# Kernel tuning notes

Measured on AMD Instinct MI355X. Metric: run time of the kernel, lower is better.

Reference implementation:

```python
import jax, jax.numpy as jnp
import numpy as np

IN_DIM = 512
HID = 512
NUM_PARENTS = 200000


def setup_inputs() -> dict:
    key = jax.random.key(0)
    k0, k1, k2, k3, k4 = jax.random.split(key, 5)
    s = 1.0 / np.sqrt(HID)
    return {
        "parent_states": jax.random.normal(k0, (NUM_PARENTS, IN_DIM), dtype=jnp.float32),
        # torch.nn.GRUCell parameters: weight_ih (3H, D), weight_hh (3H, H), biases (3H,)
        "weight_ih": jax.random.uniform(k1, (3 * HID, IN_DIM), minval=-s, maxval=s, dtype=jnp.float32),
        "weight_hh": jax.random.uniform(k2, (3 * HID, HID), minval=-s, maxval=s, dtype=jnp.float32),
        "bias_ih": jax.random.uniform(k3, (3 * HID,), minval=-s, maxval=s, dtype=jnp.float32),
        "bias_hh": jax.random.uniform(k4, (3 * HID,), minval=-s, maxval=s, dtype=jnp.float32),
    }


def reference(parent_states, weight_ih, weight_hh, bias_ih, bias_hh):
    # 1) permutation-invariant aggregation of parent states (mean)
    agg = jnp.mean(parent_states, axis=0)  # (IN_DIM,)
    # 2) GRUCell update with hx = zeros (torch GRUCell default when hx is None)
    h = jnp.zeros((HID,), dtype=parent_states.dtype)
    gi = weight_ih @ agg + bias_ih          # (3H,)
    gh = weight_hh @ h + bias_hh            # (3H,) -> just bias_hh since h=0
    gi_r, gi_z, gi_n = jnp.split(gi, 3)
    gh_r, gh_z, gh_n = jnp.split(gh, 3)
    r = jax.nn.sigmoid(gi_r + gh_r)
    z = jax.nn.sigmoid(gi_z + gh_z)
    n = jnp.tanh(gi_n + r * gh_n)
    h_new = (1.0 - z) * n + z * h           # (HID,)
    return h_new
```

## Files before the change

### kernel.cpp

```cpp
#include <hip/hip_runtime.h>
#include <math.h>

#define IN_DIM 512
#define HID 512

#define K1_BLOCKS 1024
#define K1_THREADS 256
#define K1_STRIDE (K1_BLOCKS * K1_THREADS)
#define P1 K1_BLOCKS
#define K2_BLOCKS 64
#define P2 K2_BLOCKS

__global__ __launch_bounds__(K1_THREADS) void k1_partial(const float* __restrict__ x,
                                                         float* __restrict__ part,
                                                         int total4) {
    const int gtid = blockIdx.x * K1_THREADS + threadIdx.x;
    const float4* __restrict__ x4 = (const float4*)x;
    float4 acc = make_float4(0.f, 0.f, 0.f, 0.f);
    for (int i = gtid; i < total4; i += K1_STRIDE) {
        float4 v = x4[i];
        acc.x += v.x; acc.y += v.y; acc.z += v.z; acc.w += v.w;
    }
    __shared__ float4 lds[K1_THREADS];
    lds[threadIdx.x] = acc;
    __syncthreads();
    if (threadIdx.x < 128) {
        float4 a = lds[threadIdx.x];
        float4 b = lds[threadIdx.x + 128];
        float4 s = make_float4(a.x + b.x, a.y + b.y, a.z + b.z, a.w + b.w);
        ((float4*)(part + (size_t)blockIdx.x * IN_DIM))[threadIdx.x] = s;
    }
}

__global__ __launch_bounds__(IN_DIM) void k2_reduce(const float* __restrict__ part,
                                                    float* __restrict__ part2) {
    const int j = threadIdx.x;
    const int g = blockIdx.x;
    float s = 0.f;
    const int rows = P1 / P2;
    const float* __restrict__ base = part + (size_t)g * rows * IN_DIM + j;
    for (int r = 0; r < rows; ++r) s += base[(size_t)r * IN_DIM];
    part2[(size_t)g * IN_DIM + j] = s;
}

__global__ __launch_bounds__(256) void k3_gemv_gates(const float* __restrict__ part2,
                                                     const float* __restrict__ wih,
                                                     const float* __restrict__ bih,
                                                     const float* __restrict__ bhh,
                                                     float* __restrict__ out,
                                                     float inv_n) {
    __shared__ float agg[IN_DIM];
    for (int c = threadIdx.x; c < IN_DIM; c += 256) {
        float s = 0.f;
        for (int r = 0; r < P2; ++r) s += part2[(size_t)r * IN_DIM + c];
        agg[c] = s * inv_n;
    }
    __syncthreads();

    const int w = threadIdx.x >> 6;
    const int l = threadIdx.x & 63;
    const int j = blockIdx.x * 4 + w;

    const float4* __restrict__ a4 = (const float4*)agg;
    float4 g1 = a4[l];
    float4 g2 = a4[l + 64];

    float d[3];
#pragma unroll
    for (int gidx = 0; gidx < 3; ++gidx) {
        const float4* __restrict__ w4 =
            (const float4*)(wih + (size_t)(gidx * HID + j) * IN_DIM);
        float4 w1 = w4[l];
        float4 w2 = w4[l + 64];
        d[gidx] = w1.x * g1.x + w1.y * g1.y + w1.z * g1.z + w1.w * g1.w
                + w2.x * g2.x + w2.y * g2.y + w2.z * g2.z + w2.w * g2.w;
    }

#pragma unroll
    for (int off = 32; off > 0; off >>= 1) {
        d[0] += __shfl_down(d[0], off, 64);
        d[1] += __shfl_down(d[1], off, 64);
        d[2] += __shfl_down(d[2], off, 64);
    }

    if (l == 0) {
        float gi_r = d[0] + bih[j];
        float gi_z = d[1] + bih[HID + j];
        float gi_n = d[2] + bih[2 * HID + j];
        float gh_r = bhh[j];
        float gh_z = bhh[HID + j];
        float gh_n = bhh[2 * HID + j];
        float r = 1.f / (1.f + expf(-(gi_r + gh_r)));
        float z = 1.f / (1.f + expf(-(gi_z + gh_z)));
        float n = tanhf(gi_n + r * gh_n);
        out[j] = (1.f - z) * n;
    }
}

extern "C" void kernel_launch(void* const* d_in, const int* in_sizes, int n_in,
                              void* d_out, int out_size, void* d_ws, size_t ws_size,
                              hipStream_t stream) {
    const float* x   = (const float*)d_in[0];
    const float* wih = (const float*)d_in[1];
    const float* bih = (const float*)d_in[3];
    const float* bhh = (const float*)d_in[4];
    float* out = (float*)d_out;

    const int n_par  = in_sizes[0] / IN_DIM;
    const int total4 = in_sizes[0] / 4;

    float* part  = (float*)d_ws;
    float* part2 = part + (size_t)P1 * IN_DIM;

    k1_partial<<<K1_BLOCKS, K1_THREADS, 0, stream>>>(x, part, total4);
    k2_reduce<<<K2_BLOCKS, IN_DIM, 0, stream>>>(part, part2);
    k3_gemv_gates<<<HID / 4, 256, 0, stream>>>(part2, wih, bih, bhh, out,
                                               1.0f / (float)n_par);
}
```

Baseline: 523.6 us.

## Unroll streaming reduction with nontemporal loads and double threads per block

The partial-sum kernel now uses 512 threads per block and unrolls the strided loop four ways with independent accumulators, so more loads are in flight per thread. Loads use nontemporal hints because the input is streamed only once. The block-level reduction now combines four LDS slices per column. This trades more registers per thread and a larger block for more memory-level parallelism in a bandwidth-bound pass.

```diff
diff --git a/kernel.cpp b/kernel.cpp
--- a/kernel.cpp
+++ b/kernel.cpp
@@ -5,30 +5,44 @@
 #define HID 512
 
 #define K1_BLOCKS 1024
-#define K1_THREADS 256
+#define K1_THREADS 512
 #define K1_STRIDE (K1_BLOCKS * K1_THREADS)
 #define P1 K1_BLOCKS
 #define K2_BLOCKS 64
 #define P2 K2_BLOCKS
 
+typedef float f4 __attribute__((ext_vector_type(4)));
+
 __global__ __launch_bounds__(K1_THREADS) void k1_partial(const float* __restrict__ x,
                                                          float* __restrict__ part,
                                                          int total4) {
     const int gtid = blockIdx.x * K1_THREADS + threadIdx.x;
-    const float4* __restrict__ x4 = (const float4*)x;
-    float4 acc = make_float4(0.f, 0.f, 0.f, 0.f);
-    for (int i = gtid; i < total4; i += K1_STRIDE) {
-        float4 v = x4[i];
-        acc.x += v.x; acc.y += v.y; acc.z += v.z; acc.w += v.w;
+    const f4* __restrict__ x4 = (const f4*)x;
+    f4 a0 = {0.f, 0.f, 0.f, 0.f};
+    f4 a1 = {0.f, 0.f, 0.f, 0.f};
+    f4 a2 = {0.f, 0.f, 0.f, 0.f};
+    f4 a3 = {0.f, 0.f, 0.f, 0.f};
+    int i = gtid;
+    for (; i + 3 * K1_STRIDE < total4; i += 4 * K1_STRIDE) {
+        f4 v0 = __builtin_nontemporal_load(x4 + i);
+        f4 v1 = __builtin_nontemporal_load(x4 + i + K1_STRIDE);
+        f4 v2 = __builtin_nontemporal_load(x4 + i + 2 * K1_STRIDE);
+        f4 v3 = __builtin_nontemporal_load(x4 + i + 3 * K1_STRIDE);
+        a0 += v0;
+        a1 += v1;
+        a2 += v2;
+        a3 += v3;
     }
-    __shared__ float4 lds[K1_THREADS];
+    for (; i < total4; i += K1_STRIDE) a0 += __builtin_nontemporal_load(x4 + i);
+    f4 acc = (a0 + a1) + (a2 + a3);
+
+    __shared__ f4 lds[K1_THREADS];
     lds[threadIdx.x] = acc;
     __syncthreads();
     if (threadIdx.x < 128) {
-        float4 a = lds[threadIdx.x];
-        float4 b = lds[threadIdx.x + 128];
-        float4 s = make_float4(a.x + b.x, a.y + b.y, a.z + b.z, a.w + b.w);
-        ((float4*)(part + (size_t)blockIdx.x * IN_DIM))[threadIdx.x] = s;
+        f4 s = (lds[threadIdx.x] + lds[threadIdx.x + 128]) +
+               (lds[threadIdx.x + 256] + lds[threadIdx.x + 384]);
+        ((f4*)(part + (size_t)blockIdx.x * IN_DIM))[threadIdx.x] = s;
     }
 }
 
```

Result: no change. 520.7 us (-0.6%).
